# Kernel optimization log

Measured on AMD Instinct MI355X. Metric: run time of the kernel, lower is better.

## Reference

```python
import jax, jax.numpy as jnp
import numpy as np
import math

IN_F = 4096
OUT_F = 4096
NUM_FREQ = 16
RANK = 2
N_TOK = 8192


def setup_inputs() -> dict:
    key = jax.random.key(0)
    ks = jax.random.split(key, 10)
    x = jax.random.normal(ks[0], (N_TOK, IN_F), dtype=jnp.float32)
    amp = jax.random.normal(ks[1], (NUM_FREQ,), dtype=jnp.float32) * 0.1
    rf = jax.random.normal(ks[2], (NUM_FREQ,), dtype=jnp.float32) * 2.0
    cf = jax.random.normal(ks[3], (NUM_FREQ,), dtype=jnp.float32) * 2.0
    rp = jax.random.normal(ks[4], (NUM_FREQ,), dtype=jnp.float32) * 0.5
    cp = jax.random.normal(ks[5], (NUM_FREQ,), dtype=jnp.float32) * 0.5
    lora_A = jax.random.normal(ks[6], (OUT_F, RANK), dtype=jnp.float32) * 0.01
    lora_B = jax.random.normal(ks[7], (RANK, IN_F), dtype=jnp.float32) * 0.01
    alpha = jnp.float32(0.5)
    beta = jnp.float32(0.5)
    bias = jnp.zeros((OUT_F,), dtype=jnp.float32)
    return {"x": x, "amp": amp, "rf": rf, "cf": cf, "rp": rp, "cp": cp,
            "lora_A": lora_A, "lora_B": lora_B, "alpha": alpha, "beta": beta,
            "bias": bias}


def reference(x, amp, rf, cf, rp, cp, lora_A, lora_B, alpha, beta, bias):
    out_f, in_f = lora_A.shape[0], lora_B.shape[1]
    two_pi = 2.0 * math.pi
    r = jnp.linspace(0.0, two_pi, out_f, dtype=jnp.float32)  # [out_f]
    c = jnp.linspace(0.0, two_pi, in_f, dtype=jnp.float32)   # [in_f]
    # Fourier weight synthesis: sum_k amp[k] * outer(sin(r*rf[k]+rp[k]), cos(c*cf[k]+cp[k]))
    S = jnp.sin(r[None, :] * rf[:, None] + rp[:, None])  # [nf, out_f]
    C = jnp.cos(c[None, :] * cf[:, None] + cp[:, None])  # [nf, in_f]
    W_fourier = jnp.einsum('k,ko,ki->oi', amp, S, C)     # [out_f, in_f]
    W_lora = lora_A @ lora_B                              # [out_f, in_f]
    std = math.sqrt(2.0 / (in_f + out_f))
    a = jax.nn.sigmoid(alpha)
    b = jax.nn.sigmoid(beta)
    W = a * jnp.tanh(W_fourier) * std + b * jnp.tanh(W_lora) * std
    return x @ W.T + bias
```

## Files before the change

### kernel.cpp

```cpp
#include <hip/hip_runtime.h>
#include <hip/hip_bf16.h>
#include <cstdint>

typedef __attribute__((ext_vector_type(4))) float f32x4;
typedef __attribute__((ext_vector_type(4))) int i32x4;

#define IN_F 4096
#define OUT_F 4096
#define N_TOK 8192
#define NUM_FREQ 16


__device__ inline float fast_tanh(float x) {
    float ax = fabsf(x);
    float e = __expf(2.0f * ax);
    float t = 1.0f - 2.0f / (e + 1.0f);
    return copysignf(t, x);
}

__device__ inline void load_lds16(const void* g, void* l) {
    __builtin_amdgcn_global_load_lds(
        (const __attribute__((address_space(1))) void*)(uintptr_t)g,
        (__attribute__((address_space(3))) void*)(uint32_t)(uintptr_t)l,
        16, 0, 0);
}

__device__ inline int q8(float v, float s) {
    int q = (int)rintf(v * s);
    return min(127, max(-127, q));
}

__device__ inline unsigned int pack4(int q0, int q1, int q2, int q3) {
    return (q0 & 255) | ((q1 & 255) << 8) | ((q2 & 255) << 16) |
           ((q3 & 255) << 24);
}

__global__ __launch_bounds__(256)
void prep(const float* __restrict__ x, signed char* __restrict__ xq,
          float* __restrict__ sx, const float* __restrict__ amp,
          const float* __restrict__ rf, const float* __restrict__ cf,
          const float* __restrict__ rp, const float* __restrict__ cp,
          const float* __restrict__ lA, const float* __restrict__ lB,
          const float* __restrict__ alpha, const float* __restrict__ beta,
          signed char* __restrict__ wq, float* __restrict__ sw) {
    const int tid = threadIdx.x;
    const int wave = tid >> 6;
    const int lane = tid & 63;
    __shared__ float s_s[NUM_FREQ], s_cf[NUM_FREQ], s_cp[NUM_FREQ];
    __shared__ float red[4];

    if (blockIdx.x < OUT_F) {
        const int o = blockIdx.x;
        const float step = 6.28318530717958647692f / 4095.0f;
        if (tid < NUM_FREQ) {
            float r = step * (float)o;
            s_s[tid] = amp[tid] * __sinf(r * rf[tid] + rp[tid]);
            s_cf[tid] = cf[tid];
            s_cp[tid] = cp[tid];
        }
        __syncthreads();
        const float sa = 1.0f / (1.0f + __expf(-alpha[0]));
        const float sb = 1.0f / (1.0f + __expf(-beta[0]));
        const float stdv = 0.015625f;
        const float a0 = lA[o * 2 + 0];
        const float a1 = lA[o * 2 + 1];

        float w[16];
        const int ibase = tid * 16;
        const f32x4* lB4 = (const f32x4*)lB;
#pragma unroll
        for (int g = 0; g < 4; ++g) {
            f32x4 b0 = lB4[tid * 4 + g];
            f32x4 b1 = lB4[1024 + tid * 4 + g];
#pragma unroll
            for (int e = 0; e < 4; ++e) {
                int j = g * 4 + e;
                float ci = step * (float)(ibase + j);
                float wf = 0.0f;
#pragma unroll
                for (int k = 0; k < NUM_FREQ; ++k)
                    wf += s_s[k] * __cosf(ci * s_cf[k] + s_cp[k]);
                float wl = a0 * b0[e] + a1 * b1[e];
                w[j] = sa * stdv * fast_tanh(wf) + sb * stdv * fast_tanh(wl);
            }
        }
        float m = 0.0f;
#pragma unroll
        for (int j = 0; j < 16; ++j) m = fmaxf(m, fabsf(w[j]));
#pragma unroll
        for (int off = 32; off > 0; off >>= 1)
            m = fmaxf(m, __shfl_xor(m, off));
        if (lane == 0) red[wave] = m;
        __syncthreads();
        m = fmaxf(fmaxf(red[0], red[1]), fmaxf(red[2], red[3]));
        m = fmaxf(m, 1e-20f);
        const float s = 127.0f / m;
        uint4 out;
        unsigned int* op = (unsigned int*)&out;
#pragma unroll
        for (int g = 0; g < 4; ++g)
            op[g] = pack4(q8(w[g * 4], s), q8(w[g * 4 + 1], s),
                          q8(w[g * 4 + 2], s), q8(w[g * 4 + 3], s));
        *(uint4*)(wq + (size_t)o * IN_F + ibase) = out;
        if (tid == 0) sw[o] = m / 127.0f;
    } else {
        const int t = blockIdx.x - OUT_F;
        const f32x4* xr = (const f32x4*)(x + (size_t)t * IN_F);
        f32x4 v[4];
#pragma unroll
        for (int j = 0; j < 4; ++j) v[j] = xr[tid + 256 * j];
        float m = 0.0f;
#pragma unroll
        for (int j = 0; j < 4; ++j)
#pragma unroll
            for (int e = 0; e < 4; ++e) m = fmaxf(m, fabsf(v[j][e]));
#pragma unroll
        for (int off = 32; off > 0; off >>= 1)
            m = fmaxf(m, __shfl_xor(m, off));
        if (lane == 0) red[wave] = m;
        __syncthreads();
        m = fmaxf(fmaxf(red[0], red[1]), fmaxf(red[2], red[3]));
        m = fmaxf(m, 1e-20f);
        const float s = 127.0f / m;
        unsigned int* orow = (unsigned int*)(xq + (size_t)t * IN_F);
#pragma unroll
        for (int j = 0; j < 4; ++j)
            orow[tid + 256 * j] =
                pack4(q8(v[j][0], s), q8(v[j][1], s), q8(v[j][2], s),
                      q8(v[j][3], s));
        if (tid == 0) sx[t] = m / 127.0f;
    }
}

#define BM 128
#define BN 128
#define BKB 128
#define SUBK 64

__global__ __launch_bounds__(256, 2)
void gemm_i8(const signed char* __restrict__ A, const signed char* __restrict__ B,
             const float* __restrict__ sx, const float* __restrict__ sw,
             const float* __restrict__ bias, float* __restrict__ C,
             int M, int N, int K) {
    __shared__ signed char sA[2][BM * SUBK];
    __shared__ signed char sB[2][BN * SUBK];

    const int tid = threadIdx.x;
    const int wave = tid >> 6;
    const int lane = tid & 63;

    const int bm = blockIdx.y * BM;
    const int bn = blockIdx.x * BN;

    const int srow = wave * 16 + (lane >> 2);
    const int scol = (lane & 3) * 16;

    const signed char* gA = A + (size_t)(bm + srow) * K + scol;
    const signed char* gB = B + (size_t)(bn + srow) * K + scol;

    signed char* lA0a = &sA[0][(wave * 16) * SUBK];
    signed char* lA0b = &sA[0][(64 + wave * 16) * SUBK];
    signed char* lA1a = &sA[1][(wave * 16) * SUBK];
    signed char* lA1b = &sA[1][(64 + wave * 16) * SUBK];
    signed char* lB0a = &sB[0][(wave * 16) * SUBK];
    signed char* lB0b = &sB[0][(64 + wave * 16) * SUBK];
    signed char* lB1a = &sB[1][(wave * 16) * SUBK];
    signed char* lB1b = &sB[1][(64 + wave * 16) * SUBK];

    const size_t rowK = (size_t)64 * K;

    const int wm = (wave & 1) * 64;
    const int wn = (wave >> 1) * 64;
    const int lm = lane & 15;
    const int quad = lane >> 4;

    i32x4 acc[4][4] = {};

    for (int k0 = 0; k0 < K; k0 += BKB) {
        load_lds16(gA + k0, lA0a);
        load_lds16(gA + rowK + k0, lA0b);
        load_lds16(gB + k0, lB0a);
        load_lds16(gB + rowK + k0, lB0b);
        load_lds16(gA + k0 + SUBK, lA1a);
        load_lds16(gA + rowK + k0 + SUBK, lA1b);
        load_lds16(gB + k0 + SUBK, lB1a);
        load_lds16(gB + rowK + k0 + SUBK, lB1b);
        __syncthreads();

#pragma unroll
        for (int h = 0; h < 2; ++h) {
            i32x4 af[4], bv[4];
#pragma unroll
            for (int i = 0; i < 4; ++i)
                af[i] = *(const i32x4*)&sA[h][(wm + i * 16 + lm) * SUBK +
                                             quad * 16];
#pragma unroll
            for (int i = 0; i < 4; ++i)
                bv[i] = *(const i32x4*)&sB[h][(wn + i * 16 + lm) * SUBK +
                                              quad * 16];

#pragma unroll
            for (int im = 0; im < 4; ++im)
#pragma unroll
                for (int in = 0; in < 4; ++in)
                    acc[im][in] = __builtin_amdgcn_mfma_i32_16x16x64_i8(
                        af[im], bv[in], acc[im][in], 0, 0, 0);
        }

        __syncthreads();
    }

    float sxv[4][4];
#pragma unroll
    for (int im = 0; im < 4; ++im)
#pragma unroll
        for (int r = 0; r < 4; ++r)
            sxv[im][r] = sx[bm + wm + im * 16 + quad * 4 + r];

#pragma unroll
    for (int in = 0; in < 4; ++in) {
        const int cn = bn + wn + in * 16 + lm;
        const float bv_ = bias[cn];
        const float scw = sw[cn];
#pragma unroll
        for (int im = 0; im < 4; ++im) {
            const int rm = bm + wm + im * 16 + quad * 4;
#pragma unroll
            for (int r = 0; r < 4; ++r)
                C[(size_t)(rm + r) * N + cn] =
                    (float)acc[im][in][r] * (sxv[im][r] * scw) + bv_;
        }
    }
}

extern "C" void kernel_launch(void* const* d_in, const int* in_sizes, int n_in,
                              void* d_out, int out_size, void* d_ws,
                              size_t ws_size, hipStream_t stream) {
    const float* x = (const float*)d_in[0];
    const float* amp = (const float*)d_in[1];
    const float* rf = (const float*)d_in[2];
    const float* cf = (const float*)d_in[3];
    const float* rp = (const float*)d_in[4];
    const float* cp = (const float*)d_in[5];
    const float* lA = (const float*)d_in[6];
    const float* lB = (const float*)d_in[7];
    const float* alpha = (const float*)d_in[8];
    const float* beta = (const float*)d_in[9];
    const float* bias = (const float*)d_in[10];
    float* out = (float*)d_out;

    signed char* wq = (signed char*)d_ws;
    signed char* xq = wq + (size_t)OUT_F * IN_F;
    float* sw = (float*)(xq + (size_t)N_TOK * IN_F);
    float* sx = sw + OUT_F;

    prep<<<OUT_F + N_TOK, 256, 0, stream>>>(x, xq, sx, amp, rf, cf, rp, cp,
                                            lA, lB, alpha, beta, wq, sw);
    gemm_i8<<<dim3(OUT_F / BN, N_TOK / BM), 256, 0, stream>>>(
        xq, wq, sx, sw, bias, out, N_TOK, OUT_F, IN_F);
}
```

Measured before the change: 426.6 us.

## Enlarge GEMM M-tile to 256 and swizzle LDS layout to avoid bank conflicts

Doubles the block tile in M so each wave computes a 128x64 output tile with 8x4 MFMA accumulators, which raises arithmetic intensity per LDS load of B. It also XOR-swizzles the 16-byte k-chunk position within each LDS row, both on the global-to-LDS store and on the fragment reads, to reduce LDS bank conflicts. The cost is more accumulator registers (128 VGPRs for acc) under launch_bounds(256,2), which may cause spills or lower occupancy, and the grid now has half as many blocks in M.

Result: slower. 452.2 us (+6.0%).

```diff
diff --git a/kernel.cpp b/kernel.cpp
--- a/kernel.cpp
+++ b/kernel.cpp
@@ -132,7 +132,7 @@
     }
 }
 
-#define BM 128
+#define BM 256
 #define BN 128
 #define BKB 128
 #define SUBK 64
@@ -152,55 +152,50 @@
     const int bm = blockIdx.y * BM;
     const int bn = blockIdx.x * BN;
 
-    const int srow = wave * 16 + (lane >> 2);
-    const int scol = (lane & 3) * 16;
-
-    const signed char* gA = A + (size_t)(bm + srow) * K + scol;
-    const signed char* gB = B + (size_t)(bn + srow) * K + scol;
-
-    signed char* lA0a = &sA[0][(wave * 16) * SUBK];
-    signed char* lA0b = &sA[0][(64 + wave * 16) * SUBK];
-    signed char* lA1a = &sA[1][(wave * 16) * SUBK];
-    signed char* lA1b = &sA[1][(64 + wave * 16) * SUBK];
-    signed char* lB0a = &sB[0][(wave * 16) * SUBK];
-    signed char* lB0b = &sB[0][(64 + wave * 16) * SUBK];
-    signed char* lB1a = &sB[1][(wave * 16) * SUBK];
-    signed char* lB1b = &sB[1][(64 + wave * 16) * SUBK];
-
-    const size_t rowK = (size_t)64 * K;
-
-    const int wm = (wave & 1) * 64;
-    const int wn = (wave >> 1) * 64;
+    const int srow = lane >> 2;
+    const int scol = (((lane & 3) ^ ((lane >> 3) & 3)) << 4);
+
+    const signed char* gA = A + (size_t)(bm + wave * 16 + srow) * K + scol;
+    const signed char* gB = B + (size_t)(bn + wave * 16 + srow) * K + scol;
+
     const int lm = lane & 15;
     const int quad = lane >> 4;
-
-    i32x4 acc[4][4] = {};
+    const int kq = ((quad ^ ((lm >> 1) & 3)) << 4);
+
+    const int wm = (wave & 1) * 128;
+    const int wn = (wave >> 1) * 64;
+    const int aoff = (wm + lm) * SUBK + kq;
+    const int boff = (wn + lm) * SUBK + kq;
+
+    i32x4 acc[8][4] = {};
 
     for (int k0 = 0; k0 < K; k0 += BKB) {
-        load_lds16(gA + k0, lA0a);
-        load_lds16(gA + rowK + k0, lA0b);
-        load_lds16(gB + k0, lB0a);
-        load_lds16(gB + rowK + k0, lB0b);
-        load_lds16(gA + k0 + SUBK, lA1a);
-        load_lds16(gA + rowK + k0 + SUBK, lA1b);
-        load_lds16(gB + k0 + SUBK, lB1a);
-        load_lds16(gB + rowK + k0 + SUBK, lB1b);
-        __syncthreads();
-
 #pragma unroll
         for (int h = 0; h < 2; ++h) {
-            i32x4 af[4], bv[4];
+            const int kk = k0 + h * SUBK;
+#pragma unroll
+            for (int c = 0; c < 4; ++c)
+                load_lds16(gA + (size_t)c * 64 * K + kk,
+                           &sA[h][(wave * 16 + c * 64) * SUBK]);
+#pragma unroll
+            for (int c = 0; c < 2; ++c)
+                load_lds16(gB + (size_t)c * 64 * K + kk,
+                           &sB[h][(wave * 16 + c * 64) * SUBK]);
+        }
+        __syncthreads();
+
+#pragma unroll
+        for (int h = 0; h < 2; ++h) {
+            i32x4 af[8], bv[4];
+#pragma unroll
+            for (int i = 0; i < 8; ++i)
+                af[i] = *(const i32x4*)&sA[h][aoff + i * 16 * SUBK];
 #pragma unroll
             for (int i = 0; i < 4; ++i)
-                af[i] = *(const i32x4*)&sA[h][(wm + i * 16 + lm) * SUBK +
-                                             quad * 16];
-#pragma unroll
-            for (int i = 0; i < 4; ++i)
-                bv[i] = *(const i32x4*)&sB[h][(wn + i * 16 + lm) * SUBK +
-                                              quad * 16];
-
-#pragma unroll
-            for (int im = 0; im < 4; ++im)
+                bv[i] = *(const i32x4*)&sB[h][boff + i * 16 * SUBK];
+
+#pragma unroll
+            for (int im = 0; im < 8; ++im)
 #pragma unroll
                 for (int in = 0; in < 4; ++in)
                     acc[im][in] = __builtin_amdgcn_mfma_i32_16x16x64_i8(
@@ -210,9 +205,9 @@
         __syncthreads();
     }
 
-    float sxv[4][4];
-#pragma unroll
-    for (int im = 0; im < 4; ++im)
+    float sxv[8][4];
+#pragma unroll
+    for (int im = 0; im < 8; ++im)
 #pragma unroll
         for (int r = 0; r < 4; ++r)
             sxv[im][r] = sx[bm + wm + im * 16 + quad * 4 + r];
@@ -223,7 +218,7 @@
         const float bv_ = bias[cn];
         const float scw = sw[cn];
 #pragma unroll
-        for (int im = 0; im < 4; ++im) {
+        for (int im = 0; im < 8; ++im) {
             const int rm = bm + wm + im * 16 + quad * 4;
 #pragma unroll
             for (int r = 0; r < 4; ++r)
```
